# Kernel tuning notes

Measured on AMD Instinct MI355X. Metric: run time of the kernel, lower is better.

## Reference

```python
import jax, jax.numpy as jnp
import numpy as np
from jax import lax

# Hyperparameters (match init_kwargs)
B, DIM, H, W = 8, 384, 32, 32
HEADS = 8
GROUPS = 4
OFF_SCALE = 4
K1, K2 = 5, 11  # generate_offset_kernel_sizes(4) -> [5, 11]
OFF_DIM = DIM // GROUPS  # 96
HEAD_DIM = DIM // HEADS  # 48
DN = ('NCHW', 'OIHW', 'NCHW')


def setup_inputs() -> dict:
    key = jax.random.key(0)
    ks = jax.random.split(key, 9)
    std = 0.02
    return {
        'x': jax.random.normal(ks[0], (B, DIM, H, W), jnp.float32),
        'Wq': jax.random.normal(ks[1], (DIM, DIM), jnp.float32) * std,
        'Wk': jax.random.normal(ks[2], (DIM, DIM), jnp.float32) * std,
        'Wv': jax.random.normal(ks[3], (DIM, DIM), jnp.float32) * std,
        'Wproj': jax.random.normal(ks[4], (DIM, DIM), jnp.float32) * std,
        'bproj': jnp.zeros((DIM,), jnp.float32),
        'scale': jnp.ones((1, HEADS, 1, 1), jnp.float32) / np.sqrt(HEAD_DIM),
        'Woff1': jax.random.normal(ks[5], (2, OFF_DIM, K1, K1), jnp.float32) * std,
        'Woff2': jax.random.normal(ks[6], (2, OFF_DIM, K2, K2), jnp.float32) * std,
    }


def _group(t, b, h, w):
    # 'b (h w) (g c) -> (b g) c h w'
    cg = t.shape[-1] // GROUPS
    return t.reshape(b, h, w, GROUPS, cg).transpose(0, 3, 4, 1, 2).reshape(b * GROUPS, cg, h, w)


def _ungroup(t, b, h, w):
    # '(b g) c h w -> b (h w) (g c)'
    cg = t.shape[1]
    return t.reshape(b, GROUPS, cg, h, w).transpose(0, 3, 4, 1, 2).reshape(b, h * w, GROUPS * cg)


def _bilinear(img, ys, xs):
    # img: (c, h, w); ys, xs: (h, w) absolute pixel coords -> (c, h, w)
    h, w = img.shape[1], img.shape[2]
    ys = jnp.clip(ys, 0.0, h - 1.0)
    xs = jnp.clip(xs, 0.0, w - 1.0)
    y0 = jnp.floor(ys); x0 = jnp.floor(xs)
    y0i = y0.astype(jnp.int32); x0i = x0.astype(jnp.int32)
    y1i = jnp.minimum(y0i + 1, h - 1); x1i = jnp.minimum(x0i + 1, w - 1)
    wy = ys - y0; wx = xs - x0
    g = lambda yi, xi: img[:, yi, xi]  # (c, h, w) gather
    return (g(y0i, x0i) * (1 - wy) * (1 - wx) + g(y0i, x1i) * (1 - wy) * wx
            + g(y1i, x0i) * wy * (1 - wx) + g(y1i, x1i) * wy * wx)


def reference(x, Wq, Wk, Wv, Wproj, bproj, scale, Woff1, Woff2):
    b, c, h, w = x.shape
    n = h * w
    xt = x.reshape(b, c, n).transpose(0, 2, 1)  # b n c
    q = xt @ Wq.T  # b n c

    # Offset generator: per-group multi-scale convs -> tanh-bounded offsets scaled by offset_scale
    qg = _group(q, b, h, w)  # (b*g, off_dim, h, w)
    off = (lax.conv_general_dilated(qg, Woff1, (1, 1), 'SAME', dimension_numbers=DN)
           + lax.conv_general_dilated(qg, Woff2, (1, 1), 'SAME', dimension_numbers=DN))
    offsets = jnp.tanh(off) * OFF_SCALE  # (b*g, 2, h, w)

    # apply_offsets: bilinear gather of grouped x at base grid + offsets
    xg = _group(xt, b, h, w)  # (b*g, off_dim, h, w)
    by, bx = jnp.meshgrid(jnp.arange(h, dtype=jnp.float32), jnp.arange(w, dtype=jnp.float32), indexing='ij')
    ys = by[None] + offsets[:, 0]
    xs = bx[None] + offsets[:, 1]
    kv = jax.vmap(_bilinear)(xg, ys, xs)  # (b*g, off_dim, h, w)
    kvf = _ungroup(kv, b, h, w)  # b n c

    k = kvf @ Wk.T
    v = kvf @ Wv.T
    heads = lambda t: t.reshape(b, n, HEADS, HEAD_DIM).transpose(0, 2, 1, 3)  # b h n d
    qh, kh, vh = heads(q), heads(k), heads(v)

    attn = jnp.einsum('bhid,bhjd->bhij', qh, kh) * scale  # learnable per-head scale
    attn = jax.nn.softmax(attn, axis=-1)
    out = jnp.einsum('bhij,bhjd->bhid', attn, vh)  # b h n d
    out = out.transpose(0, 2, 1, 3).reshape(b, n, c)
    out = out @ Wproj.T + bproj
    return out.transpose(0, 2, 1).reshape(b, c, h, w)
```

## Files before the change

kernel.cpp:

```cpp
#include <hip/hip_runtime.h>
#include <hip/hip_bf16.h>

#define DIMC 384
#define NHEADS 8
#define HDIM 48
#define OFFD 96
#define NPIX 1024
#define BB 8

typedef short bf16s;
typedef __attribute__((ext_vector_type(8))) short short8;
typedef __attribute__((ext_vector_type(4))) float f32x4;

__device__ __forceinline__ short f2b(float f) {
  union { float f; unsigned u; } v; v.f = f;
  unsigned r = (v.u + 0x7fffu + ((v.u >> 16) & 1u)) >> 16;
  return (short)r;
}
__device__ __forceinline__ float b2f(short s) {
  union { unsigned u; float f; } v; v.u = ((unsigned)(unsigned short)s) << 16; return v.f;
}
__device__ __forceinline__ unsigned pk2(float a, float b) {
  union { __hip_bfloat162 h; unsigned u; } v;
  v.h = __float22bfloat162_rn(float2{a, b});
  return v.u;
}

__global__ __launch_bounds__(256) void prep_weights(
    const float* __restrict__ Wq, const float* __restrict__ Wk,
    const float* __restrict__ Wv, const float* __restrict__ Wp,
    bf16s* __restrict__ wqh, bf16s* __restrict__ wql,
    bf16s* __restrict__ wkb, bf16s* __restrict__ wvb, bf16s* __restrict__ wpb) {
  int idx = blockIdx.x * 256 + threadIdx.x;
  if (idx >= 4 * 147456) return;
  int which = idx / 147456, e = idx % 147456;
  if (which == 0) {
    float v = Wq[e]; short h = f2b(v);
    wqh[e] = h; wql[e] = f2b(v - b2f(h));
  } else if (which == 1) wkb[e] = f2b(Wk[e]);
  else if (which == 2) wvb[e] = f2b(Wv[e]);
  else wpb[e] = f2b(Wp[e]);
}

__global__ __launch_bounds__(256) void transpose_split(const float* __restrict__ x,
    bf16s* __restrict__ xh, bf16s* __restrict__ xl) {
  __shared__ float ts[64][65];
  int np0 = blockIdx.x * 64, c0 = blockIdx.y * 64, b = blockIdx.z;
  int t = threadIdx.x;
  int a = t & 63, bq = t >> 6;
#pragma unroll
  for (int i = 0; i < 16; ++i) {
    int cl = bq + i * 4;
    ts[cl][a] = x[((size_t)(b * DIMC + c0 + cl)) * NPIX + np0 + a];
  }
  __syncthreads();
#pragma unroll
  for (int i = 0; i < 16; ++i) {
    int npl = bq + i * 4;
    float v = ts[a][npl];
    short h = f2b(v);
    size_t o = ((size_t)(b * NPIX + np0 + npl)) * DIMC + c0 + a;
    xh[o] = h; xl[o] = f2b(v - b2f(h));
  }
}

template<int MODE>
__global__ __launch_bounds__(256) void gemm_lds(
    const bf16s* __restrict__ Ah, const bf16s* __restrict__ Al,
    const bf16s* __restrict__ Wa, const bf16s* __restrict__ Wb,
    float* __restrict__ outF, bf16s* __restrict__ outB, bf16s* __restrict__ outB2,
    const float* __restrict__ bias) {
  __shared__ __align__(16) short wlds[25600];
  const int NS  = (MODE == 2) ? 1 : 2;
  const int KCN = (MODE == 2) ? 48 : 24;
  const int STR = (MODE == 2) ? 392 : 200;
  int t = threadIdx.x;
  int w = t >> 6, lane = t & 63, quad = lane >> 4, l16 = lane & 15;
  int n0 = blockIdx.x * 64;
  int m0 = blockIdx.y * 64 + w * 16;
  f32x4 acc[4], acc2[4];
#pragma unroll
  for (int nt = 0; nt < 4; ++nt) {
    acc[nt] = (f32x4){0.f, 0.f, 0.f, 0.f};
    if (MODE != 2) acc2[nt] = (f32x4){0.f, 0.f, 0.f, 0.f};
  }
  const bf16s* arow_a = Ah + (size_t)(m0 + l16) * DIMC;
  const bf16s* arow_l = (MODE == 0) ? (Al + (size_t)(m0 + l16) * DIMC) : nullptr;

  for (int s = 0; s < NS; ++s) {
    if (s) __syncthreads();
    int kcb = s * 24;
#pragma unroll
    for (int ii = 0; ii < (KCN * 64) / 256; ++ii) {
      int i = ii * 256 + t;
      int n = i / KCN, kcl = i % KCN;
      *(short8*)(&wlds[n * STR + kcl * 8]) =
          *(const short8*)(Wa + (size_t)(n0 + n) * DIMC + (kcb + kcl) * 8);
      if (MODE != 2)
        *(short8*)(&wlds[12800 + n * STR + kcl * 8]) =
            *(const short8*)(Wb + (size_t)(n0 + n) * DIMC + (kcb + kcl) * 8);
    }
    __syncthreads();
    int k0beg = s * 6, k0cnt = (MODE == 2) ? 12 : 6;
#pragma unroll
    for (int kk = 0; kk < k0cnt; ++kk) {
      int k0 = k0beg + kk;
      short8 a0 = *(const short8*)(arow_a + k0 * 32 + quad * 8);
      short8 a1;
      if (MODE == 0) a1 = *(const short8*)(arow_l + k0 * 32 + quad * 8);
      int kcl = kk * 4 + quad;
#pragma unroll
      for (int nt = 0; nt < 4; ++nt) {
        int n = nt * 16 + l16;
        short8 b0 = *(const short8*)(&wlds[n * STR + kcl * 8]);
        acc[nt] = __builtin_amdgcn_mfma_f32_16x16x32_bf16(a0, b0, acc[nt], 0, 0, 0);
        if (MODE == 0) {
          short8 b1 = *(const short8*)(&wlds[12800 + n * STR + kcl * 8]);
          acc[nt] = __builtin_amdgcn_mfma_f32_16x16x32_bf16(a1, b0, acc[nt], 0, 0, 0);
          acc[nt] = __builtin_amdgcn_mfma_f32_16x16x32_bf16(a0, b1, acc[nt], 0, 0, 0);
        } else if (MODE == 1) {
          short8 b1 = *(const short8*)(&wlds[12800 + n * STR + kcl * 8]);
          acc2[nt] = __builtin_amdgcn_mfma_f32_16x16x32_bf16(a0, b1, acc2[nt], 0, 0, 0);
        }
      }
    }
  }
#pragma unroll
  for (int nt = 0; nt < 4; ++nt) {
    int c = n0 + nt * 16 + l16;
#pragma unroll
    for (int r = 0; r < 4; ++r) {
      int m = m0 + quad * 4 + r;
      int b = m >> 10, np = m & 1023;
      float v = acc[nt][r];
      if (MODE == 0) {
        int g = c / OFFD, cc = c % OFFD;
        outF[((size_t)((b * 4 + g) * OFFD + cc)) * NPIX + np] = v;
        int h = c / HDIM, d = c % HDIM;
        outB[((size_t)((b * 8 + h) * NPIX + np)) * HDIM + d] = f2b(v);
      } else if (MODE == 1) {
        int h = c / HDIM, d = c % HDIM;
        outB[((size_t)((b * 8 + h) * NPIX + np)) * HDIM + d] = f2b(v);
        outB2[((size_t)((b * 8 + h) * HDIM + d)) * NPIX + np] = f2b(acc2[nt][r]);
      } else {
        outF[((size_t)(b * DIMC + c)) * NPIX + np] = v + bias[c];
      }
    }
  }
}

__global__ __launch_bounds__(256) void conv_off_part(const float* __restrict__ qg,
    const float* __restrict__ W1, const float* __restrict__ W2, float* __restrict__ pbuf) {
  __shared__ float ts[42 * 43];
  int chunk = blockIdx.x & 15, bg = blockIdx.x >> 4;
  int t = threadIdx.x;
  int y = t >> 3, x0 = (t & 7) * 4;
  float a0[4] = {0.f, 0.f, 0.f, 0.f}, a1[4] = {0.f, 0.f, 0.f, 0.f};
  const float* plane0 = qg + (size_t)bg * OFFD * NPIX;
  for (int ci = 0; ci < 6; ++ci) {
    int cc = chunk * 6 + ci;
    const float* plane = plane0 + (size_t)cc * NPIX;
    __syncthreads();
    for (int e = t; e < 42 * 42; e += 256) {
      int r = e / 42, c = e - r * 42;
      int gy = r - 5, gx = c - 5;
      ts[r * 43 + c] = (gy >= 0 && gy < 32 && gx >= 0 && gx < 32) ? plane[gy * 32 + gx] : 0.f;
    }
    __syncthreads();
    const float* w1c0 = W1 + (size_t)cc * 25;
    const float* w1c1 = W1 + (size_t)(OFFD + cc) * 25;
    const float* w2c0 = W2 + (size_t)cc * 121;
    const float* w2c1 = W2 + (size_t)(OFFD + cc) * 121;
#pragma unroll
    for (int ky = 0; ky < 11; ++ky) {
      float rv[14];
#pragma unroll
      for (int j = 0; j < 14; ++j) rv[j] = ts[(y + ky) * 43 + x0 + j];
#pragma unroll
      for (int kx = 0; kx < 11; ++kx) {
        float w0 = w2c0[ky * 11 + kx], w1v = w2c1[ky * 11 + kx];
#pragma unroll
        for (int o = 0; o < 4; ++o) {
          a0[o] = fmaf(rv[kx + o], w0, a0[o]);
          a1[o] = fmaf(rv[kx + o], w1v, a1[o]);
        }
      }
    }
#pragma unroll
    for (int ky = 0; ky < 5; ++ky) {
      float rv[8];
#pragma unroll
      for (int j = 0; j < 8; ++j) rv[j] = ts[(y + ky + 3) * 43 + x0 + 3 + j];
#pragma unroll
      for (int kx = 0; kx < 5; ++kx) {
        float w0 = w1c0[ky * 5 + kx], w1v = w1c1[ky * 5 + kx];
#pragma unroll
        for (int o = 0; o < 4; ++o) {
          a0[o] = fmaf(rv[kx + o], w0, a0[o]);
          a1[o] = fmaf(rv[kx + o], w1v, a1[o]);
        }
      }
    }
  }
  float* pb = pbuf + ((size_t)(chunk * 32 + bg) * 2) * NPIX;
#pragma unroll
  for (int o = 0; o < 4; ++o) {
    int n = y * 32 + x0 + o;
    pb[n] = a0[o];
    pb[NPIX + n] = a1[o];
  }
}

__global__ __launch_bounds__(256) void conv_off_reduce(const float* __restrict__ pbuf,
                                                       float* __restrict__ offs) {
  int idx = blockIdx.x * 256 + threadIdx.x;
  float s = 0.f;
#pragma unroll
  for (int ch = 0; ch < 16; ++ch) s += pbuf[(size_t)ch * 65536 + idx];
  offs[idx] = tanhf(s) * 4.0f;
}

__global__ __launch_bounds__(256) void bilinear_kernel(const float* __restrict__ x,
    const float* __restrict__ offs, bf16s* __restrict__ kvf) {
  int chunk = blockIdx.x & 7, ntile = (blockIdx.x >> 3) & 3, bg = blockIdx.x >> 5;
  int n = ntile * 256 + threadIdx.x;
  int b = bg >> 2, g = bg & 3;
  int iy = n >> 5, ix = n & 31;
  float ys = (float)iy + offs[(size_t)bg * 2 * NPIX + n];
  float xs = (float)ix + offs[(size_t)bg * 2 * NPIX + NPIX + n];
  ys = fminf(fmaxf(ys, 0.f), 31.f);
  xs = fminf(fmaxf(xs, 0.f), 31.f);
  float y0f = floorf(ys), x0f = floorf(xs);
  int y0 = (int)y0f, x0 = (int)x0f;
  int y1 = min(y0 + 1, 31), x1 = min(x0 + 1, 31);
  float wy = ys - y0f, wx = xs - x0f;
  float w00 = (1.f - wy) * (1.f - wx), w01 = (1.f - wy) * wx;
  float w10 = wy * (1.f - wx), w11 = wy * wx;
  const float* xp = x + ((size_t)b * DIMC + g * OFFD + chunk * 12) * NPIX;
  bf16s* out = kvf + (size_t)(b * 1024 + n) * DIMC + g * OFFD + chunk * 12;
  int i00 = y0 * 32 + x0, i01 = y0 * 32 + x1, i10 = y1 * 32 + x0, i11 = y1 * 32 + x1;
#pragma unroll
  for (int cc = 0; cc < 12; ++cc) {
    const float* pl = xp + (size_t)cc * NPIX;
    out[cc] = f2b(w00 * pl[i00] + w01 * pl[i01] + w10 * pl[i10] + w11 * pl[i11]);
  }
}

__global__ __launch_bounds__(256) void flash_attn_kernel(
    const bf16s* __restrict__ qb, const bf16s* __restrict__ kb,
    const bf16s* __restrict__ vt, const float* __restrict__ scale,
    bf16s* __restrict__ out) {
  __shared__ short Ps[4][2][16 * 140];
  int tid = threadIdx.x;
  int w = tid >> 6, lane = tid & 63;
  int quad = lane >> 4, l16 = lane & 15;
  int qt = blockIdx.x >> 6, bh = blockIdx.x & 63;
  int b = bh >> 3, h = bh & 7;
  int q0 = qt * 64 + w * 16;
  float sc = scale[h] * 1.44269504f;

  const bf16s* qbase = qb + (size_t)bh * NPIX * HDIM;
  const bf16s* kbase = kb + (size_t)bh * NPIX * HDIM;
  const bf16s* vbase = vt + (size_t)bh * HDIM * NPIX;

  short8 bq0, bq1;
  {
    const bf16s* qrow = qbase + (size_t)(q0 + l16) * HDIM;
    short8 r0 = *(const short8*)(qrow + quad * 8);
    short8 r1;
    if (quad < 2) r1 = *(const short8*)(qrow + 32 + quad * 8);
    else { short8 z = {0,0,0,0,0,0,0,0}; r1 = z; }
#pragma unroll
    for (int j = 0; j < 8; ++j) {
      bq0[j] = f2b(b2f(r0[j]) * sc);
      bq1[j] = f2b(b2f(r1[j]) * sc);
    }
  }
  float l_run = 0.f;
  f32x4 O[3];
#pragma unroll
  for (int nt = 0; nt < 3; ++nt) O[nt] = (f32x4){0.f, 0.f, 0.f, 0.f};

#pragma unroll 2
  for (int kt = 0; kt < 8; ++kt) {
    int key0 = kt * 128;
    short* ps = &Ps[w][kt & 1][0];
    f32x4 Sv[8];
#pragma unroll
    for (int s = 0; s < 2; ++s)
#pragma unroll
      for (int nt = 0; nt < 4; ++nt) {
        const bf16s* krow = kbase + (size_t)(key0 + s * 64 + nt * 16 + l16) * HDIM;
        short8 ak0 = *(const short8*)(krow + quad * 8);
        short8 ak1;
        if (quad < 2) ak1 = *(const short8*)(krow + 32 + quad * 8);
        else { short8 z = {0,0,0,0,0,0,0,0}; ak1 = z; }
        f32x4 acc = (f32x4){0.f, 0.f, 0.f, 0.f};
        acc = __builtin_amdgcn_mfma_f32_16x16x32_bf16(ak0, bq0, acc, 0, 0, 0);
        acc = __builtin_amdgcn_mfma_f32_16x16x32_bf16(ak1, bq1, acc, 0, 0, 0);
        Sv[s * 4 + nt] = acc;
      }
    float ls0 = 0.f, ls1 = 0.f, ls2 = 0.f, ls3 = 0.f;
#pragma unroll
    for (int i = 0; i < 8; i += 4) {
#pragma unroll
      for (int r = 0; r < 4; ++r) {
        float p0 = __builtin_amdgcn_exp2f(Sv[i][r]);
        float p1 = __builtin_amdgcn_exp2f(Sv[i + 1][r]);
        float p2 = __builtin_amdgcn_exp2f(Sv[i + 2][r]);
        float p3 = __builtin_amdgcn_exp2f(Sv[i + 3][r]);
        Sv[i][r] = p0; Sv[i + 1][r] = p1; Sv[i + 2][r] = p2; Sv[i + 3][r] = p3;
        ls0 += p0; ls1 += p1; ls2 += p2; ls3 += p3;
      }
    }
    float ls = (ls0 + ls1) + (ls2 + ls3);
    ls += __shfl_xor(ls, 16, 64);
    ls += __shfl_xor(ls, 32, 64);
    l_run += ls;
#pragma unroll
    for (int s = 0; s < 2; ++s)
#pragma unroll
      for (int nt = 0; nt < 4; ++nt) {
        uint2 pk;
        pk.x = pk2(Sv[s * 4 + nt][0], Sv[s * 4 + nt][1]);
        pk.y = pk2(Sv[s * 4 + nt][2], Sv[s * 4 + nt][3]);
        *(uint2*)(ps + l16 * 140 + s * 64 + nt * 16 + quad * 4) = pk;
      }
#pragma unroll
    for (int ks = 0; ks < 4; ++ks) {
      short8 ap = *(short8*)(ps + l16 * 140 + ks * 32 + quad * 8);
#pragma unroll
      for (int nt = 0; nt < 3; ++nt) {
        const bf16s* vrow = vbase + (size_t)(nt * 16 + l16) * NPIX + key0 + ks * 32;
        short8 bv = *(const short8*)(vrow + quad * 8);
        O[nt] = __builtin_amdgcn_mfma_f32_16x16x32_bf16(ap, bv, O[nt], 0, 0, 0);
      }
    }
  }
#pragma unroll
  for (int r = 0; r < 4; ++r) {
    float lr = __shfl(l_run, quad * 4 + r, 64);
    float inv = 1.0f / lr;
    int qrow = q0 + quad * 4 + r;
    bf16s* orow = out + ((size_t)(b * 1024 + qrow)) * DIMC + h * HDIM;
#pragma unroll
    for (int nt = 0; nt < 3; ++nt) orow[nt * 16 + l16] = f2b(O[nt][r] * inv);
  }
}

extern "C" void kernel_launch(void* const* d_in, const int* in_sizes, int n_in,
                              void* d_out, int out_size, void* d_ws, size_t ws_size,
                              hipStream_t stream) {
  const float* x  = (const float*)d_in[0];
  const float* Wq = (const float*)d_in[1];
  const float* Wk = (const float*)d_in[2];
  const float* Wv = (const float*)d_in[3];
  const float* Wp = (const float*)d_in[4];
  const float* bp = (const float*)d_in[5];
  const float* sc = (const float*)d_in[6];
  const float* W1 = (const float*)d_in[7];
  const float* W2 = (const float*)d_in[8];
  float* ws = (float*)d_ws;
  const size_t S = (size_t)BB * NPIX * DIMC;
  float* qg   = ws;
  float* offs = ws + S;
  float* pbuf = ws + S + 65536;
  bf16s* sb   = (bf16s*)(ws + S + 65536 + 1048576);
  bf16s* xh   = sb;
  bf16s* xl   = sb + S;
  bf16s* qbuf = sb + 2 * S;
  bf16s* kvfb = sb + 3 * S;
  bf16s* wqh  = sb + 4 * S;
  bf16s* wql  = wqh + 147456;
  bf16s* wkb  = wql + 147456;
  bf16s* wvb  = wkb + 147456;
  bf16s* wpb  = wvb + 147456;
  bf16s* attnout = (bf16s*)qg;
  bf16s* kbuf = xh;
  bf16s* vbuf = xl;

  prep_weights<<<2304, 256, 0, stream>>>(Wq, Wk, Wv, Wp, wqh, wql, wkb, wvb, wpb);
  transpose_split<<<dim3(16, 6, BB), 256, 0, stream>>>(x, xh, xl);
  gemm_lds<0><<<dim3(6, 128), 256, 0, stream>>>(xh, xl, wqh, wql, qg, qbuf, nullptr, nullptr);
  conv_off_part<<<512, 256, 0, stream>>>(qg, W1, W2, pbuf);
  conv_off_reduce<<<256, 256, 0, stream>>>(pbuf, offs);
  bilinear_kernel<<<1024, 256, 0, stream>>>(x, offs, kvfb);
  gemm_lds<1><<<dim3(6, 128), 256, 0, stream>>>(kvfb, nullptr, wkb, wvb, nullptr, kbuf, vbuf, nullptr);
  flash_attn_kernel<<<1024, 256, 0, stream>>>(qbuf, kbuf, vbuf, sc, attnout);
  gemm_lds<2><<<dim3(6, 128), 256, 0, stream>>>(attnout, nullptr, wpb, nullptr, (float*)d_out, nullptr, nullptr, bp);
}
```

Measured before the change: 249.5 us.

## Split flash attention keys across warps and pad Q/K rows to 64

The attention kernel now launches twice as many blocks, each covering 32 queries, with the four warps split into two query halves and two key halves. The key-half partial outputs and row sums are combined through shared memory after a block barrier. Q and K are stored with a 64-element padded row stride, zeroed by memsets before use, so each lane can load without the quad<2 branch. This trades extra memset traffic, padded memory reads and a cross-warp reduction for more parallelism and fewer divergent loads.

```diff
diff --git a/kernel.cpp b/kernel.cpp
--- a/kernel.cpp
+++ b/kernel.cpp
@@ -137,10 +137,10 @@
         int g = c / OFFD, cc = c % OFFD;
         outF[((size_t)((b * 4 + g) * OFFD + cc)) * NPIX + np] = v;
         int h = c / HDIM, d = c % HDIM;
-        outB[((size_t)((b * 8 + h) * NPIX + np)) * HDIM + d] = f2b(v);
+        outB[((size_t)((b * 8 + h) * NPIX + np)) * 64 + d] = f2b(v);
       } else if (MODE == 1) {
         int h = c / HDIM, d = c % HDIM;
-        outB[((size_t)((b * 8 + h) * NPIX + np)) * HDIM + d] = f2b(v);
+        outB[((size_t)((b * 8 + h) * NPIX + np)) * 64 + d] = f2b(v);
         outB2[((size_t)((b * 8 + h) * HDIM + d)) * NPIX + np] = f2b(acc2[nt][r]);
       } else {
         outF[((size_t)(b * DIMC + c)) * NPIX + np] = v + bias[c];
@@ -246,30 +246,29 @@
   }
 }
 
-__global__ __launch_bounds__(256) void flash_attn_kernel(
+__global__ __launch_bounds__(256, 8) void flash_attn_kernel(
     const bf16s* __restrict__ qb, const bf16s* __restrict__ kb,
     const bf16s* __restrict__ vt, const float* __restrict__ scale,
     bf16s* __restrict__ out) {
-  __shared__ short Ps[4][2][16 * 140];
+  __shared__ short Ps[4][16 * 140];
   int tid = threadIdx.x;
   int w = tid >> 6, lane = tid & 63;
   int quad = lane >> 4, l16 = lane & 15;
-  int qt = blockIdx.x >> 6, bh = blockIdx.x & 63;
+  int bh = blockIdx.x & 63, qt32 = blockIdx.x >> 6;
   int b = bh >> 3, h = bh & 7;
-  int q0 = qt * 64 + w * 16;
+  int q0 = qt32 * 32 + (w & 1) * 16;
+  int khalf = w >> 1;
   float sc = scale[h] * 1.44269504f;
 
-  const bf16s* qbase = qb + (size_t)bh * NPIX * HDIM;
-  const bf16s* kbase = kb + (size_t)bh * NPIX * HDIM;
+  const bf16s* qbase = qb + (size_t)bh * NPIX * 64;
+  const bf16s* kbase = kb + (size_t)bh * NPIX * 64;
   const bf16s* vbase = vt + (size_t)bh * HDIM * NPIX;
 
   short8 bq0, bq1;
   {
-    const bf16s* qrow = qbase + (size_t)(q0 + l16) * HDIM;
+    const bf16s* qrow = qbase + (size_t)(q0 + l16) * 64;
     short8 r0 = *(const short8*)(qrow + quad * 8);
-    short8 r1;
-    if (quad < 2) r1 = *(const short8*)(qrow + 32 + quad * 8);
-    else { short8 z = {0,0,0,0,0,0,0,0}; r1 = z; }
+    short8 r1 = *(const short8*)(qrow + 32 + quad * 8);
 #pragma unroll
     for (int j = 0; j < 8; ++j) {
       bq0[j] = f2b(b2f(r0[j]) * sc);
@@ -280,21 +279,19 @@
   f32x4 O[3];
 #pragma unroll
   for (int nt = 0; nt < 3; ++nt) O[nt] = (f32x4){0.f, 0.f, 0.f, 0.f};
-
-#pragma unroll 2
-  for (int kt = 0; kt < 8; ++kt) {
-    int key0 = kt * 128;
-    short* ps = &Ps[w][kt & 1][0];
+  short* ps = &Ps[w][0];
+
+#pragma unroll 1
+  for (int kt = 0; kt < 4; ++kt) {
+    int key0 = khalf * 512 + kt * 128;
     f32x4 Sv[8];
 #pragma unroll
     for (int s = 0; s < 2; ++s)
 #pragma unroll
       for (int nt = 0; nt < 4; ++nt) {
-        const bf16s* krow = kbase + (size_t)(key0 + s * 64 + nt * 16 + l16) * HDIM;
+        const bf16s* krow = kbase + (size_t)(key0 + s * 64 + nt * 16 + l16) * 64;
         short8 ak0 = *(const short8*)(krow + quad * 8);
-        short8 ak1;
-        if (quad < 2) ak1 = *(const short8*)(krow + 32 + quad * 8);
-        else { short8 z = {0,0,0,0,0,0,0,0}; ak1 = z; }
+        short8 ak1 = *(const short8*)(krow + 32 + quad * 8);
         f32x4 acc = (f32x4){0.f, 0.f, 0.f, 0.f};
         acc = __builtin_amdgcn_mfma_f32_16x16x32_bf16(ak0, bq0, acc, 0, 0, 0);
         acc = __builtin_amdgcn_mfma_f32_16x16x32_bf16(ak1, bq1, acc, 0, 0, 0);
@@ -337,14 +334,31 @@
       }
     }
   }
-#pragma unroll
-  for (int r = 0; r < 4; ++r) {
-    float lr = __shfl(l_run, quad * 4 + r, 64);
-    float inv = 1.0f / lr;
-    int qrow = q0 + quad * 4 + r;
-    bf16s* orow = out + ((size_t)(b * 1024 + qrow)) * DIMC + h * HDIM;
-#pragma unroll
-    for (int nt = 0; nt < 3; ++nt) orow[nt * 16 + l16] = f2b(O[nt][r] * inv);
+  if (w >= 2) {
+    float* xb = (float*)ps;
+#pragma unroll
+    for (int nt = 0; nt < 3; ++nt)
+#pragma unroll
+      for (int r = 0; r < 4; ++r) xb[lane * 13 + nt * 4 + r] = O[nt][r];
+    xb[lane * 13 + 12] = l_run;
+  }
+  __syncthreads();
+  if (w < 2) {
+    const float* src = (const float*)&Ps[w + 2][0];
+#pragma unroll
+    for (int nt = 0; nt < 3; ++nt)
+#pragma unroll
+      for (int r = 0; r < 4; ++r) O[nt][r] += src[lane * 13 + nt * 4 + r];
+    l_run += src[lane * 13 + 12];
+#pragma unroll
+    for (int r = 0; r < 4; ++r) {
+      float lr = __shfl(l_run, quad * 4 + r, 64);
+      float inv = 1.0f / lr;
+      int qrow = q0 + quad * 4 + r;
+      bf16s* orow = out + ((size_t)(b * 1024 + qrow)) * DIMC + h * HDIM;
+#pragma unroll
+      for (int nt = 0; nt < 3; ++nt) orow[nt * 16 + l16] = f2b(O[nt][r] * inv);
+    }
   }
 }
 
@@ -362,6 +376,7 @@
   const float* W2 = (const float*)d_in[8];
   float* ws = (float*)d_ws;
   const size_t S = (size_t)BB * NPIX * DIMC;
+  const size_t SP = (size_t)64 * NPIX * 64;
   float* qg   = ws;
   float* offs = ws + S;
   float* pbuf = ws + S + 65536;
@@ -369,23 +384,25 @@
   bf16s* xh   = sb;
   bf16s* xl   = sb + S;
   bf16s* qbuf = sb + 2 * S;
-  bf16s* kvfb = sb + 3 * S;
-  bf16s* wqh  = sb + 4 * S;
+  bf16s* kvfb = qbuf + SP;
+  bf16s* vbuf = kvfb + S;
+  bf16s* wqh  = vbuf + S;
   bf16s* wql  = wqh + 147456;
   bf16s* wkb  = wql + 147456;
   bf16s* wvb  = wkb + 147456;
   bf16s* wpb  = wvb + 147456;
   bf16s* attnout = (bf16s*)qg;
   bf16s* kbuf = xh;
-  bf16s* vbuf = xl;
-
+
+  hipMemsetAsync(qbuf, 0, SP * sizeof(bf16s), stream);
   prep_weights<<<2304, 256, 0, stream>>>(Wq, Wk, Wv, Wp, wqh, wql, wkb, wvb, wpb);
   transpose_split<<<dim3(16, 6, BB), 256, 0, stream>>>(x, xh, xl);
   gemm_lds<0><<<dim3(6, 128), 256, 0, stream>>>(xh, xl, wqh, wql, qg, qbuf, nullptr, nullptr);
+  hipMemsetAsync(kbuf, 0, SP * sizeof(bf16s), stream);
   conv_off_part<<<512, 256, 0, stream>>>(qg, W1, W2, pbuf);
   conv_off_reduce<<<256, 256, 0, stream>>>(pbuf, offs);
   bilinear_kernel<<<1024, 256, 0, stream>>>(x, offs, kvfb);
   gemm_lds<1><<<dim3(6, 128), 256, 0, stream>>>(kvfb, nullptr, wkb, wvb, nullptr, kbuf, vbuf, nullptr);
-  flash_attn_kernel<<<1024, 256, 0, stream>>>(qbuf, kbuf, vbuf, sc, attnout);
+  flash_attn_kernel<<<2048, 256, 0, stream>>>(qbuf, kbuf, vbuf, sc, attnout);
   gemm_lds<2><<<dim3(6, 128), 256, 0, stream>>>(attnout, nullptr, wpb, nullptr, (float*)d_out, nullptr, nullptr, bp);
 }
```

New measurement: 307.1 us. 1.23x slower.
